# Performance work log

Measured on AMD Instinct MI355X. Metric: run time of the kernel, lower is better.

Reference implementation:

```python
import jax, jax.numpy as jnp
import numpy as np

B, N, D, E, H, K = 2, 2048, 1024, 8, 2048, 2


def setup_inputs() -> dict:
    key = jax.random.key(0)
    ks = jax.random.split(key, 5)
    s = 0.02  # init scale
    return {
        "x": jax.random.normal(ks[0], (B, N, D), dtype=jnp.float32),
        "w_gate": jax.random.normal(ks[1], (D, E), dtype=jnp.float32) * s,
        "b_gate": jnp.zeros((E,), dtype=jnp.float32),
        "w1": jax.random.normal(ks[2], (E, D, H), dtype=jnp.float32) * s,
        "b1": jnp.zeros((E, H), dtype=jnp.float32),
        "w2": jax.random.normal(ks[3], (E, H, D), dtype=jnp.float32) * s,
        "b2": jnp.zeros((E, D), dtype=jnp.float32),
    }


def reference(x, w_gate, b_gate, w1, b1, w2, b2):
    b, n, d = x.shape
    T = b * n
    xf = x.reshape(T, d)                                   # (T, D)
    # --- top-k routing ---
    logits = xf @ w_gate + b_gate                          # (T, E)
    topk_logits, topk_idx = jax.lax.top_k(logits, K)       # (T, K)
    topk_gates = jax.nn.softmax(topk_logits, axis=-1)      # softmax over selected experts
    entropy = -(topk_gates * jnp.log(jnp.clip(topk_gates, 1e-8, None))).sum(-1).mean()
    # scatter top-k gates into full (T, E) gate matrix (zeros for unselected)
    gates = jnp.zeros_like(logits).at[jnp.arange(T)[:, None], topk_idx].add(topk_gates)
    # --- expert MLPs (dense over experts; gates zero out unselected) ---
    h = jax.nn.relu(jnp.einsum('td,edh->eth', xf, w1) + b1[:, None, :])  # (E, T, H)
    y = jnp.einsum('eth,ehd->etd', h, w2) + b2[:, None, :]               # (E, T, D)
    out = jnp.einsum('etd,te->td', y, gates).reshape(b, n, d)
    return out, entropy
```

## Files before the change

kernel.cpp:

```cpp
#include <hip/hip_runtime.h>

#define T_TOK 4096
#define D_DIM 1024
#define E_EXP 8
#define H_DIM 2048
#define CAP   9216
#define TILES_M 72

typedef __attribute__((ext_vector_type(8))) short bf16x8;
typedef __attribute__((ext_vector_type(4))) float f32x4;

__device__ inline unsigned short f2bf(float f) {
    unsigned int u = __float_as_uint(f);
    unsigned int r = (u + 0x7fffu + ((u >> 16) & 1u)) >> 16;
    return (unsigned short)r;
}

#define GLD_LDS16(g, l)                                                        \
    __builtin_amdgcn_global_load_lds(                                          \
        (const __attribute__((address_space(1))) void*)(g),                    \
        (__attribute__((address_space(3))) void*)(l), 16, 0, 0)

__global__ __launch_bounds__(256) void tcvt_kernel(const float* __restrict__ src,
                                                   unsigned short* __restrict__ dst,
                                                   int R, int C) {
    __shared__ float tile[64][65];
    size_t eo = (size_t)blockIdx.z * R * C;
    src += eo; dst += eo;
    int tx = threadIdx.x & 15, ty = threadIdx.x >> 4;
    int c0 = blockIdx.x * 64, r0 = blockIdx.y * 64;
    #pragma unroll
    for (int i = 0; i < 4; i++) {
        int row = ty + i * 16;
        float4 v = *(const float4*)&src[(size_t)(r0 + row) * C + c0 + tx * 4];
        tile[row][tx * 4 + 0] = v.x;
        tile[row][tx * 4 + 1] = v.y;
        tile[row][tx * 4 + 2] = v.z;
        tile[row][tx * 4 + 3] = v.w;
    }
    __syncthreads();
    #pragma unroll
    for (int i = 0; i < 4; i++) {
        int cc = ty + i * 16;
        int rr = tx * 4;
        ushort4 o;
        o.x = f2bf(tile[rr + 0][cc]);
        o.y = f2bf(tile[rr + 1][cc]);
        o.z = f2bf(tile[rr + 2][cc]);
        o.w = f2bf(tile[rr + 3][cc]);
        *(ushort4*)&dst[(size_t)(c0 + cc) * R + r0 + rr] = o;
    }
}

__global__ __launch_bounds__(256) void gating_kernel(
    const float* __restrict__ xf, const float* __restrict__ wg,
    const float* __restrict__ bg, unsigned short* __restrict__ xb,
    int* __restrict__ tk_e, float* __restrict__ tk_g,
    float* __restrict__ ent_part)
{
    __shared__ float ents[4];
    int wave = threadIdx.x >> 6, lane = threadIdx.x & 63;
    int t = blockIdx.x * 4 + wave;
    const float* xr = xf + (size_t)t * D_DIM;
    unsigned short* xbr = xb + (size_t)t * D_DIM;
    float acc[8] = {0.f,0.f,0.f,0.f,0.f,0.f,0.f,0.f};
    for (int i = 0; i < 16; i++) {
        int d = lane + i * 64;
        float xv = xr[d];
        xbr[d] = f2bf(xv);
        const float4* wr = (const float4*)(wg + (size_t)d * 8);
        float4 w0 = wr[0], w1 = wr[1];
        acc[0] += xv * w0.x; acc[1] += xv * w0.y; acc[2] += xv * w0.z; acc[3] += xv * w0.w;
        acc[4] += xv * w1.x; acc[5] += xv * w1.y; acc[6] += xv * w1.z; acc[7] += xv * w1.w;
    }
    #pragma unroll
    for (int s = 1; s < 64; s <<= 1) {
        #pragma unroll
        for (int e = 0; e < 8; e++) acc[e] += __shfl_xor(acc[e], s, 64);
    }
    if (lane == 0) {
        float l[8];
        #pragma unroll
        for (int e = 0; e < 8; e++) l[e] = acc[e] + bg[e];
        int i0 = 0;
        #pragma unroll
        for (int e = 1; e < 8; e++) if (l[e] > l[i0]) i0 = e;
        int i1 = (i0 == 0) ? 1 : 0;
        #pragma unroll
        for (int e = 0; e < 8; e++) if (e != i0 && l[e] > l[i1]) i1 = e;
        float z  = expf(l[i1] - l[i0]);
        float p0 = 1.0f / (1.0f + z);
        float p1 = z / (1.0f + z);
        float ent = -(p0 * logf(fmaxf(p0, 1e-8f)) + p1 * logf(fmaxf(p1, 1e-8f)));
        ents[wave] = ent;
        tk_e[t * 2 + 0] = i0; tk_g[t * 2 + 0] = p0;
        tk_e[t * 2 + 1] = i1; tk_g[t * 2 + 1] = p1;
    }
    __syncthreads();
    if (threadIdx.x == 0)
        ent_part[blockIdx.x] = ents[0] + ents[1] + ents[2] + ents[3];
}

__global__ __launch_bounds__(1024) void route_kernel(
    const int* __restrict__ tk_e, const float* __restrict__ tk_g,
    int* __restrict__ off, int* __restrict__ slot_token,
    float* __restrict__ slot_gate, int* __restrict__ slot_of,
    const float* __restrict__ ent_part, float* __restrict__ ent_out)
{
    __shared__ int wt[16][8];
    __shared__ int wx[16][8];
    __shared__ int base[9];
    __shared__ int tot[8];
    __shared__ float es[16];

    int tid = threadIdx.x, wid = tid >> 6, lane = tid & 63;
    int i0 = tid * 8;
    int ev[8];
    *(int4*)&ev[0] = *(const int4*)&tk_e[i0];
    *(int4*)&ev[4] = *(const int4*)&tk_e[i0 + 4];

    float s = ent_part[tid];
    #pragma unroll
    for (int d = 1; d < 64; d <<= 1) s += __shfl_xor(s, d, 64);
    if (lane == 0) es[wid] = s;

    unsigned own[4] = {0u, 0u, 0u, 0u};
    #pragma unroll
    for (int j = 0; j < 8; j++) {
        int e = ev[j];
        int reg = ((e < 4) ? 0 : 2) + (e & 1);
        own[reg] += 1u << (((e >> 1) & 1) * 16);
    }
    unsigned inc[4] = {own[0], own[1], own[2], own[3]};
    #pragma unroll
    for (int d = 1; d < 64; d <<= 1) {
        #pragma unroll
        for (int k = 0; k < 4; k++) {
            unsigned t = __shfl_up(inc[k], d, 64);
            if (lane >= d) inc[k] += t;
        }
    }
    if (lane == 63) {
        #pragma unroll
        for (int e = 0; e < 8; e++) {
            int reg = ((e < 4) ? 0 : 2) + (e & 1);
            wt[wid][e] = (inc[reg] >> (((e >> 1) & 1) * 16)) & 0xFFFF;
        }
    }
    __syncthreads();
    if (tid == 0) {
        int o = 0;
        for (int e = 0; e < 8; e++) {
            int run = 0;
            for (int w = 0; w < 16; w++) { wx[w][e] = run; run += wt[w][e]; }
            tot[e] = run;
            base[e] = o;
            off[e] = o;
            o += (run + 127) & ~127;
        }
        base[8] = o;
        off[8] = o;
        float se = 0.f;
        for (int w = 0; w < 16; w++) se += es[w];
        *ent_out = se * (1.0f / T_TOK);
    }
    __syncthreads();

    #pragma unroll
    for (int e = 0; e < 8; e++) {
        int p0 = base[e] + tot[e], p1 = base[e + 1];
        for (int i = p0 + tid; i < p1; i += 1024) slot_token[i] = -1;
    }

    unsigned run[4] = {0u, 0u, 0u, 0u};
    #pragma unroll
    for (int j = 0; j < 8; j++) {
        int e = ev[j];
        int reg = ((e < 4) ? 0 : 2) + (e & 1);
        int sh = ((e >> 1) & 1) * 16;
        int lx = (int)(((inc[reg] - own[reg]) >> sh) & 0xFFFF);
        int lr = (int)((run[reg] >> sh) & 0xFFFF);
        int slot = base[e] + wx[wid][e] + lx + lr;
        run[reg] += 1u << sh;
        int i = i0 + j;
        slot_token[slot] = i >> 1;
        slot_gate[slot] = tk_g[i];
        slot_of[i] = slot;
    }
}

template<int KD, int ND, bool GATHER, bool RELU>
__global__ __launch_bounds__(256, 2) void gemmk_kernel(
    const unsigned short* __restrict__ Ag, const unsigned short* __restrict__ Bw,
    const float* __restrict__ bias, const int* __restrict__ off,
    const int* __restrict__ slot_token, unsigned short* __restrict__ Out)
{
    constexpr int NT = KD / 64;
    __shared__ __align__(16) unsigned short As[2][128 * 64];
    __shared__ __align__(16) unsigned short Bs[2][128 * 64];

    int s0 = blockIdx.x * 128;
    if (s0 >= off[E_EXP]) return;
    int e = 0;
    while (s0 >= off[e + 1]) e++;
    int n0 = blockIdx.y * 128;

    int tid = threadIdx.x;
    int w = tid >> 6, lane = tid & 63;
    int wm = w >> 1, wn = w & 1;
    int lrow = lane & 15, quad = lane >> 4;

    int gchunk = ((lane & 7) ^ (lane >> 3)) * 8;
    const unsigned short* ap[4];
    const unsigned short* bp[4];
    const unsigned short* wbp = Bw + (size_t)e * ND * KD;
    #pragma unroll
    for (int i = 0; i < 4; i++) {
        int row = i * 32 + w * 8 + (lane >> 3);
        if constexpr (GATHER) {
            int t0 = slot_token[s0 + row]; if (t0 < 0) t0 = 0;
            ap[i] = Ag + (size_t)t0 * KD + gchunk;
        } else {
            ap[i] = Ag + (size_t)(s0 + row) * KD + gchunk;
        }
        bp[i] = wbp + (size_t)(n0 + row) * KD + gchunk;
    }

    f32x4 acc[4][4];
    #pragma unroll
    for (int mi = 0; mi < 4; mi++)
        #pragma unroll
        for (int ni = 0; ni < 4; ni++) acc[mi][ni] = (f32x4){0.f, 0.f, 0.f, 0.f};

    auto STAGE = [&](int b, int ku) {
        int koff = ku * 64;
        #pragma unroll
        for (int i = 0; i < 4; i++) {
            GLD_LDS16(ap[i] + koff, &As[b][i * 2048 + w * 512]);
            GLD_LDS16(bp[i] + koff, &Bs[b][i * 2048 + w * 512]);
        }
    };

    auto COMPUTE = [&](int b) {
        bf16x8 af[4][2], bfr[4][2];
        #pragma unroll
        for (int mi = 0; mi < 4; mi++) {
            int row = wm * 64 + mi * 16 + lrow;
            int rb = row * 64, sw = row & 7;
            af[mi][0] = *(const bf16x8*)&As[b][rb + ((quad    ) ^ sw) * 8];
            af[mi][1] = *(const bf16x8*)&As[b][rb + ((quad + 4) ^ sw) * 8];
        }
        #pragma unroll
        for (int ni = 0; ni < 4; ni++) {
            int row = wn * 64 + ni * 16 + lrow;
            int rb = row * 64, sw = row & 7;
            bfr[ni][0] = *(const bf16x8*)&Bs[b][rb + ((quad    ) ^ sw) * 8];
            bfr[ni][1] = *(const bf16x8*)&Bs[b][rb + ((quad + 4) ^ sw) * 8];
        }
        __builtin_amdgcn_s_setprio(1);
        #pragma unroll
        for (int ks = 0; ks < 2; ks++)
            #pragma unroll
            for (int mi = 0; mi < 4; mi++)
                #pragma unroll
                for (int ni = 0; ni < 4; ni++)
                    acc[mi][ni] = __builtin_amdgcn_mfma_f32_16x16x32_bf16(
                        af[mi][ks], bfr[ni][ks], acc[mi][ni], 0, 0, 0);
        __builtin_amdgcn_s_setprio(0);
    };

    STAGE(0, 0);
    STAGE(1, 1);
    for (int t = 0; t < NT - 1; ++t) {
        asm volatile("s_waitcnt vmcnt(8)" ::: "memory");
        asm volatile("s_barrier" ::: "memory");
        COMPUTE(t & 1);
        asm volatile("s_barrier" ::: "memory");
        if (t + 2 < NT) STAGE(t & 1, t + 2);
    }
    asm volatile("s_waitcnt vmcnt(0)" ::: "memory");
    asm volatile("s_barrier" ::: "memory");
    COMPUTE((NT - 1) & 1);
    asm volatile("s_barrier" ::: "memory");

    int wr = wm * 64, wc = wn * 64;
    float bv[4];
    #pragma unroll
    for (int ni = 0; ni < 4; ni++)
        bv[ni] = bias[(size_t)e * ND + n0 + wc + ni * 16 + lrow];
    unsigned short* scr = &As[0][0] + w * 1024;
    #pragma unroll
    for (int mi = 0; mi < 4; mi++) {
        #pragma unroll
        for (int ni = 0; ni < 4; ni++)
            #pragma unroll
            for (int rr = 0; rr < 4; rr++) {
                float v = acc[mi][ni][rr] + bv[ni];
                if constexpr (RELU) v = fmaxf(v, 0.0f);
                scr[(quad * 4 + rr) * 64 + ni * 16 + lrow] = f2bf(v);
            }
        int rd = lane >> 3, cc = (lane & 7) * 8;
        bf16x8 v0 = *(const bf16x8*)&scr[rd * 64 + cc];
        bf16x8 v1 = *(const bf16x8*)&scr[(8 + rd) * 64 + cc];
        size_t rowg = (size_t)(s0 + wr + mi * 16 + rd) * ND + n0 + wc + cc;
        *(bf16x8*)&Out[rowg] = v0;
        *(bf16x8*)&Out[rowg + 8 * (size_t)ND] = v1;
    }
}

__global__ __launch_bounds__(256) void combine_kernel(
    const unsigned short* __restrict__ Yb, const int* __restrict__ slot_of,
    const float* __restrict__ tk_g, float* __restrict__ out)
{
    int t = blockIdx.x * 2 + (threadIdx.x >> 7);
    int j = threadIdx.x & 127;
    int sA = slot_of[t * 2], sB = slot_of[t * 2 + 1];
    float gA = tk_g[t * 2], gB = tk_g[t * 2 + 1];
    uint4 va = *(const uint4*)(Yb + (size_t)sA * D_DIM + j * 8);
    uint4 vb = *(const uint4*)(Yb + (size_t)sB * D_DIM + j * 8);
    const unsigned int* pa = (const unsigned int*)&va;
    const unsigned int* pb = (const unsigned int*)&vb;
    float o[8];
    #pragma unroll
    for (int i = 0; i < 4; i++) {
        float a_lo = __uint_as_float(pa[i] << 16);
        float a_hi = __uint_as_float(pa[i] & 0xffff0000u);
        float b_lo = __uint_as_float(pb[i] << 16);
        float b_hi = __uint_as_float(pb[i] & 0xffff0000u);
        o[i * 2 + 0] = gA * a_lo + gB * b_lo;
        o[i * 2 + 1] = gA * a_hi + gB * b_hi;
    }
    float* op = out + (size_t)t * D_DIM + j * 8;
    ((float4*)op)[0] = make_float4(o[0], o[1], o[2], o[3]);
    ((float4*)op)[1] = make_float4(o[4], o[5], o[6], o[7]);
}

extern "C" void kernel_launch(void* const* d_in, const int* in_sizes, int n_in,
                              void* d_out, int out_size, void* d_ws, size_t ws_size,
                              hipStream_t stream)
{
    const float* xf = (const float*)d_in[0];
    const float* wg = (const float*)d_in[1];
    const float* bg = (const float*)d_in[2];
    const float* w1 = (const float*)d_in[3];
    const float* b1 = (const float*)d_in[4];
    const float* w2 = (const float*)d_in[5];
    const float* b2 = (const float*)d_in[6];
    float* out = (float*)d_out;

    char* p = (char*)d_ws;
    int* off    = (int*)p;
    int* tk_e   = off + 16;
    float* tk_g = (float*)(tk_e + T_TOK * 2);
    int* slot_token = (int*)(tk_g + T_TOK * 2);
    float* slot_gate = (float*)(slot_token + CAP);
    int* slot_of = (int*)(slot_gate + CAP);
    float* ent_part = (float*)(slot_of + T_TOK * 2);
    size_t ofs = ((size_t)((char*)(ent_part + T_TOK / 4) - p) + 255) & ~(size_t)255;
    unsigned short* xb  = (unsigned short*)(p + ofs); ofs += (size_t)T_TOK * D_DIM * 2;
    unsigned short* w1t = (unsigned short*)(p + ofs); ofs += (size_t)E_EXP * D_DIM * H_DIM * 2;
    unsigned short* w2t = (unsigned short*)(p + ofs); ofs += (size_t)E_EXP * H_DIM * D_DIM * 2;
    unsigned short* Hb  = (unsigned short*)(p + ofs); ofs += (size_t)CAP * H_DIM * 2;
    unsigned short* Yb  = w1t;

    gating_kernel<<<T_TOK / 4, 256, 0, stream>>>(xf, wg, bg, xb, tk_e, tk_g, ent_part);
    route_kernel<<<1, 1024, 0, stream>>>(tk_e, tk_g, off, slot_token, slot_gate, slot_of,
                                         ent_part, out + (size_t)T_TOK * D_DIM);
    tcvt_kernel<<<dim3(H_DIM / 64, D_DIM / 64, E_EXP), 256, 0, stream>>>(w1, w1t, D_DIM, H_DIM);
    tcvt_kernel<<<dim3(D_DIM / 64, H_DIM / 64, E_EXP), 256, 0, stream>>>(w2, w2t, H_DIM, D_DIM);
    gemmk_kernel<D_DIM, H_DIM, true, true>
        <<<dim3(TILES_M, H_DIM / 128), 256, 0, stream>>>(xb, w1t, b1, off, slot_token, Hb);
    gemmk_kernel<H_DIM, D_DIM, false, false>
        <<<dim3(TILES_M, D_DIM / 128), 256, 0, stream>>>(Hb, w2t, b2, off, slot_token, Yb);
    combine_kernel<<<T_TOK / 2, 256, 0, stream>>>(Yb, slot_of, tk_g, out);
}
```

Baseline: 336.7 us.

## Switch expert GEMMs to 256x256 tiles with 8 waves and interleaved staging

Both expert GEMMs now use a 256x256 output tile per 512-thread block instead of 128x128 per 256 threads, raising operand reuse from LDS. Each K-step is split into four sub-blocks that interleave global-to-LDS staging with MFMA work. Routing pads each expert's slot range to 256 instead of 128, and capacity grows to match. The cost is more padded rows computed, a larger LDS footprint, and fewer blocks per GEMM, especially the second GEMM with only 160 blocks, which may leave CUs idle.

```diff
diff --git a/kernel.cpp b/kernel.cpp
--- a/kernel.cpp
+++ b/kernel.cpp
@@ -4,8 +4,8 @@
 #define D_DIM 1024
 #define E_EXP 8
 #define H_DIM 2048
-#define CAP   9216
-#define TILES_M 72
+#define CAP   10240
+#define TILES_M 40
 
 typedef __attribute__((ext_vector_type(8))) short bf16x8;
 typedef __attribute__((ext_vector_type(4))) float f32x4;
@@ -156,7 +156,7 @@
             tot[e] = run;
             base[e] = o;
             off[e] = o;
-            o += (run + 127) & ~127;
+            o += (run + 255) & ~255;
         }
         base[8] = o;
         off[8] = o;
@@ -190,107 +190,157 @@
 }
 
 template<int KD, int ND, bool GATHER, bool RELU>
-__global__ __launch_bounds__(256, 2) void gemmk_kernel(
+__global__ __launch_bounds__(512, 2) void gemm256_kernel(
     const unsigned short* __restrict__ Ag, const unsigned short* __restrict__ Bw,
     const float* __restrict__ bias, const int* __restrict__ off,
     const int* __restrict__ slot_token, unsigned short* __restrict__ Out)
 {
     constexpr int NT = KD / 64;
-    __shared__ __align__(16) unsigned short As[2][128 * 64];
-    __shared__ __align__(16) unsigned short Bs[2][128 * 64];
-
-    int s0 = blockIdx.x * 128;
+    __shared__ __align__(16) unsigned short As[2][16384];
+    __shared__ __align__(16) unsigned short Bs[2][16384];
+
+    int s0 = blockIdx.x * 256;
     if (s0 >= off[E_EXP]) return;
     int e = 0;
     while (s0 >= off[e + 1]) e++;
-    int n0 = blockIdx.y * 128;
+    int n0 = blockIdx.y * 256;
 
     int tid = threadIdx.x;
     int w = tid >> 6, lane = tid & 63;
-    int wm = w >> 1, wn = w & 1;
+    int wm = w >> 2, wn = w & 3;
     int lrow = lane & 15, quad = lane >> 4;
 
     int gchunk = ((lane & 7) ^ (lane >> 3)) * 8;
-    const unsigned short* ap[4];
-    const unsigned short* bp[4];
+    int rw0 = w * 16 + (lane >> 3);
+    int rw1 = rw0 + 8;
+
+    const unsigned short* aP00; const unsigned short* aP01;
+    const unsigned short* aP10; const unsigned short* aP11;
+    if constexpr (GATHER) {
+        int t00 = slot_token[s0 + rw0];        if (t00 < 0) t00 = 0;
+        int t01 = slot_token[s0 + rw1];        if (t01 < 0) t01 = 0;
+        int t10 = slot_token[s0 + 128 + rw0];  if (t10 < 0) t10 = 0;
+        int t11 = slot_token[s0 + 128 + rw1];  if (t11 < 0) t11 = 0;
+        aP00 = Ag + (size_t)t00 * KD + gchunk;
+        aP01 = Ag + (size_t)t01 * KD + gchunk;
+        aP10 = Ag + (size_t)t10 * KD + gchunk;
+        aP11 = Ag + (size_t)t11 * KD + gchunk;
+    } else {
+        aP00 = Ag + (size_t)(s0 + rw0) * KD + gchunk;
+        aP01 = Ag + (size_t)(s0 + rw1) * KD + gchunk;
+        aP10 = Ag + (size_t)(s0 + 128 + rw0) * KD + gchunk;
+        aP11 = Ag + (size_t)(s0 + 128 + rw1) * KD + gchunk;
+    }
     const unsigned short* wbp = Bw + (size_t)e * ND * KD;
-    #pragma unroll
-    for (int i = 0; i < 4; i++) {
-        int row = i * 32 + w * 8 + (lane >> 3);
-        if constexpr (GATHER) {
-            int t0 = slot_token[s0 + row]; if (t0 < 0) t0 = 0;
-            ap[i] = Ag + (size_t)t0 * KD + gchunk;
+    const unsigned short* bP00 = wbp + (size_t)(n0 + rw0) * KD + gchunk;
+    const unsigned short* bP01 = wbp + (size_t)(n0 + rw1) * KD + gchunk;
+    const unsigned short* bP10 = wbp + (size_t)(n0 + 128 + rw0) * KD + gchunk;
+    const unsigned short* bP11 = wbp + (size_t)(n0 + 128 + rw1) * KD + gchunk;
+
+#define STAGE_A(BB, H, TT)                                                     \
+    { GLD_LDS16(aP##H##0 + (TT) * 64, &As[BB][((H) * 128 + w * 16) * 64]);     \
+      GLD_LDS16(aP##H##1 + (TT) * 64, &As[BB][((H) * 128 + w * 16 + 8) * 64]); }
+#define STAGE_B(BB, H, TT)                                                     \
+    { GLD_LDS16(bP##H##0 + (TT) * 64, &Bs[BB][((H) * 128 + w * 16) * 64]);     \
+      GLD_LDS16(bP##H##1 + (TT) * 64, &Bs[BB][((H) * 128 + w * 16 + 8) * 64]); }
+
+#define LDA(B, QM, AF)                                                         \
+    _Pragma("unroll") for (int i_ = 0; i_ < 4; i_++) {                         \
+        int row_ = wm * 128 + ((QM) * 4 + i_) * 16 + lrow;                     \
+        int sw_ = lrow & 7;                                                    \
+        int rb_ = row_ * 64;                                                   \
+        AF[i_][0] = *(const bf16x8*)&As[B][rb_ + ((quad    ) ^ sw_) * 8];      \
+        AF[i_][1] = *(const bf16x8*)&As[B][rb_ + ((quad + 4) ^ sw_) * 8];      \
+    }
+#define LDB(B, QN, BF)                                                         \
+    _Pragma("unroll") for (int j_ = 0; j_ < 2; j_++) {                         \
+        int row_ = wn * 64 + ((QN) * 2 + j_) * 16 + lrow;                      \
+        int sw_ = lrow & 7;                                                    \
+        int rb_ = row_ * 64;                                                   \
+        BF[j_][0] = *(const bf16x8*)&Bs[B][rb_ + ((quad    ) ^ sw_) * 8];      \
+        BF[j_][1] = *(const bf16x8*)&Bs[B][rb_ + ((quad + 4) ^ sw_) * 8];      \
+    }
+#define MM16(AF, BF, MB, NB)                                                   \
+    __builtin_amdgcn_s_setprio(1);                                             \
+    _Pragma("unroll") for (int ks_ = 0; ks_ < 2; ks_++)                        \
+    _Pragma("unroll") for (int i_ = 0; i_ < 4; i_++)                           \
+    _Pragma("unroll") for (int j_ = 0; j_ < 2; j_++)                           \
+        acc[(MB) + i_][(NB) + j_] = __builtin_amdgcn_mfma_f32_16x16x32_bf16(   \
+            AF[i_][ks_], BF[j_][ks_], acc[(MB) + i_][(NB) + j_], 0, 0, 0);     \
+    __builtin_amdgcn_s_setprio(0);
+#define BAR asm volatile("s_barrier" ::: "memory")
+
+#define DO_TILE(B, SA0, SA1, SB0, SB1, GATE)                                   \
+    {                                                                          \
+        bf16x8 af[4][2], b01[2][2], b23[2][2];                                 \
+                                                  \
+        LDA(B, 0, af); LDB(B, 0, b01);                                         \
+        SA0;                                                                   \
+        BAR;                                                                   \
+        MM16(af, b01, 0, 0);                                                   \
+        BAR;                                                                   \
+                                                  \
+        LDB(B, 1, b23);                                                        \
+        SA1;                                                                   \
+        BAR;                                                                   \
+        MM16(af, b23, 0, 2);                                                   \
+        BAR;                                                                   \
+                                                  \
+        LDA(B, 1, af);                                                         \
+        SB0;                                                                   \
+        BAR;                                                                   \
+        MM16(af, b23, 4, 2);                                                   \
+        BAR;                                                                   \
+                                                  \
+        SB1;                                                                   \
+        BAR;                                                                   \
+        MM16(af, b01, 4, 0);                                                   \
+        GATE;                                                                  \
+        BAR;                                                                   \
+    }
+
+    f32x4 acc[8][4];
+    #pragma unroll
+    for (int mi = 0; mi < 8; mi++)
+        #pragma unroll
+        for (int ni = 0; ni < 4; ni++) acc[mi][ni] = (f32x4){0.f, 0.f, 0.f, 0.f};
+
+    STAGE_B(0, 0, 0); STAGE_B(0, 1, 0);
+    STAGE_A(0, 0, 0); STAGE_A(0, 1, 0);
+    STAGE_B(1, 0, 1); STAGE_B(1, 1, 1);
+    asm volatile("s_waitcnt vmcnt(4)" ::: "memory");
+    BAR;
+
+    for (int tt = 0; tt < NT; ++tt) {
+        int b = tt & 1;
+        if (tt < NT - 2) {
+            DO_TILE(b,
+                STAGE_A(b ^ 1, 0, tt + 1), STAGE_A(b ^ 1, 1, tt + 1),
+                STAGE_B(b, 0, tt + 2),     STAGE_B(b, 1, tt + 2),
+                asm volatile("s_waitcnt vmcnt(4)" ::: "memory"));
+        } else if (tt == NT - 2) {
+            DO_TILE(b,
+                STAGE_A(b ^ 1, 0, tt + 1), STAGE_A(b ^ 1, 1, tt + 1),
+                , ,
+                asm volatile("s_waitcnt vmcnt(0)" ::: "memory"));
         } else {
-            ap[i] = Ag + (size_t)(s0 + row) * KD + gchunk;
+            DO_TILE(b, , , , , );
         }
-        bp[i] = wbp + (size_t)(n0 + row) * KD + gchunk;
-    }
-
-    f32x4 acc[4][4];
-    #pragma unroll
-    for (int mi = 0; mi < 4; mi++)
-        #pragma unroll
-        for (int ni = 0; ni < 4; ni++) acc[mi][ni] = (f32x4){0.f, 0.f, 0.f, 0.f};
-
-    auto STAGE = [&](int b, int ku) {
-        int koff = ku * 64;
-        #pragma unroll
-        for (int i = 0; i < 4; i++) {
-            GLD_LDS16(ap[i] + koff, &As[b][i * 2048 + w * 512]);
-            GLD_LDS16(bp[i] + koff, &Bs[b][i * 2048 + w * 512]);
-        }
-    };
-
-    auto COMPUTE = [&](int b) {
-        bf16x8 af[4][2], bfr[4][2];
-        #pragma unroll
-        for (int mi = 0; mi < 4; mi++) {
-            int row = wm * 64 + mi * 16 + lrow;
-            int rb = row * 64, sw = row & 7;
-            af[mi][0] = *(const bf16x8*)&As[b][rb + ((quad    ) ^ sw) * 8];
-            af[mi][1] = *(const bf16x8*)&As[b][rb + ((quad + 4) ^ sw) * 8];
-        }
-        #pragma unroll
-        for (int ni = 0; ni < 4; ni++) {
-            int row = wn * 64 + ni * 16 + lrow;
-            int rb = row * 64, sw = row & 7;
-            bfr[ni][0] = *(const bf16x8*)&Bs[b][rb + ((quad    ) ^ sw) * 8];
-            bfr[ni][1] = *(const bf16x8*)&Bs[b][rb + ((quad + 4) ^ sw) * 8];
-        }
-        __builtin_amdgcn_s_setprio(1);
-        #pragma unroll
-        for (int ks = 0; ks < 2; ks++)
-            #pragma unroll
-            for (int mi = 0; mi < 4; mi++)
-                #pragma unroll
-                for (int ni = 0; ni < 4; ni++)
-                    acc[mi][ni] = __builtin_amdgcn_mfma_f32_16x16x32_bf16(
-                        af[mi][ks], bfr[ni][ks], acc[mi][ni], 0, 0, 0);
-        __builtin_amdgcn_s_setprio(0);
-    };
-
-    STAGE(0, 0);
-    STAGE(1, 1);
-    for (int t = 0; t < NT - 1; ++t) {
-        asm volatile("s_waitcnt vmcnt(8)" ::: "memory");
-        asm volatile("s_barrier" ::: "memory");
-        COMPUTE(t & 1);
-        asm volatile("s_barrier" ::: "memory");
-        if (t + 2 < NT) STAGE(t & 1, t + 2);
-    }
-    asm volatile("s_waitcnt vmcnt(0)" ::: "memory");
-    asm volatile("s_barrier" ::: "memory");
-    COMPUTE((NT - 1) & 1);
-    asm volatile("s_barrier" ::: "memory");
-
-    int wr = wm * 64, wc = wn * 64;
+    }
+#undef DO_TILE
+#undef MM16
+#undef LDA
+#undef LDB
+#undef STAGE_A
+#undef STAGE_B
+
     float bv[4];
     #pragma unroll
     for (int ni = 0; ni < 4; ni++)
-        bv[ni] = bias[(size_t)e * ND + n0 + wc + ni * 16 + lrow];
+        bv[ni] = bias[(size_t)e * ND + n0 + wn * 64 + ni * 16 + lrow];
     unsigned short* scr = &As[0][0] + w * 1024;
     #pragma unroll
-    for (int mi = 0; mi < 4; mi++) {
+    for (int mi = 0; mi < 8; mi++) {
         #pragma unroll
         for (int ni = 0; ni < 4; ni++)
             #pragma unroll
@@ -302,7 +352,7 @@
         int rd = lane >> 3, cc = (lane & 7) * 8;
         bf16x8 v0 = *(const bf16x8*)&scr[rd * 64 + cc];
         bf16x8 v1 = *(const bf16x8*)&scr[(8 + rd) * 64 + cc];
-        size_t rowg = (size_t)(s0 + wr + mi * 16 + rd) * ND + n0 + wc + cc;
+        size_t rowg = (size_t)(s0 + wm * 128 + mi * 16 + rd) * ND + n0 + wn * 64 + cc;
         *(bf16x8*)&Out[rowg] = v0;
         *(bf16x8*)&Out[rowg + 8 * (size_t)ND] = v1;
     }
@@ -368,9 +418,9 @@
                                          ent_part, out + (size_t)T_TOK * D_DIM);
     tcvt_kernel<<<dim3(H_DIM / 64, D_DIM / 64, E_EXP), 256, 0, stream>>>(w1, w1t, D_DIM, H_DIM);
     tcvt_kernel<<<dim3(D_DIM / 64, H_DIM / 64, E_EXP), 256, 0, stream>>>(w2, w2t, H_DIM, D_DIM);
-    gemmk_kernel<D_DIM, H_DIM, true, true>
-        <<<dim3(TILES_M, H_DIM / 128), 256, 0, stream>>>(xb, w1t, b1, off, slot_token, Hb);
-    gemmk_kernel<H_DIM, D_DIM, false, false>
-        <<<dim3(TILES_M, D_DIM / 128), 256, 0, stream>>>(Hb, w2t, b2, off, slot_token, Yb);
+    gemm256_kernel<D_DIM, H_DIM, true, true>
+        <<<dim3(TILES_M, H_DIM / 256), 512, 0, stream>>>(xb, w1t, b1, off, slot_token, Hb);
+    gemm256_kernel<H_DIM, D_DIM, false, false>
+        <<<dim3(TILES_M, D_DIM / 256), 512, 0, stream>>>(Hb, w2t, b2, off, slot_token, Yb);
     combine_kernel<<<T_TOK / 2, 256, 0, stream>>>(Yb, slot_of, tk_g, out);
 }
```

Result: slower. 829.9 us (+146.5%).
